# Kernel optimization log

Measured on AMD Instinct MI355X. Metric: run time of the kernel, lower is better.

The kernel has to match this reference:

```python
import jax, jax.numpy as jnp
import numpy as np

H = 256    # hidden_size
NH = 8     # num_heads
B = 256    # batch_size (num graphs)
M = 128    # max_num_nodes per graph
N = B * M  # total nodes
E = N * 16 # total edges


def _bn(x, g, b, eps=1e-5):
    # BatchNorm1d in training mode: batch stats over node dim, biased variance
    m = x.mean(0)
    v = ((x - m) ** 2).mean(0)
    return g * (x - m) * jax.lax.rsqrt(v + eps) + b


def setup_inputs() -> dict:
    key = jax.random.key(0)
    ks = jax.random.split(key, 12)
    def lin(k, o, i):
        return jax.random.normal(k, (o, i), jnp.float32) / np.sqrt(i).astype(np.float32)
    return {
        "h": jax.random.normal(ks[0], (N, H), jnp.float32),
        "gin_w1": lin(ks[1], H, H), "gin_b1": jnp.zeros((H,), jnp.float32),
        "gin_w2": lin(ks[2], H, H), "gin_b2": jnp.zeros((H,), jnp.float32),
        "in_proj_w": lin(ks[3], 3 * H, H), "in_proj_b": jnp.zeros((3 * H,), jnp.float32),
        "out_proj_w": lin(ks[4], H, H), "out_proj_b": jnp.zeros((H,), jnp.float32),
        "bn_local_g": jnp.ones((H,), jnp.float32), "bn_local_b": jnp.zeros((H,), jnp.float32),
        "bn_attn_g": jnp.ones((H,), jnp.float32), "bn_attn_b": jnp.zeros((H,), jnp.float32),
        "bn_out_g": jnp.ones((H,), jnp.float32), "bn_out_b": jnp.zeros((H,), jnp.float32),
        "ffn1_w": lin(ks[5], 2 * H, H), "ffn1_b": jnp.zeros((2 * H,), jnp.float32),
        "ffn2_w": lin(ks[6], H, 2 * H), "ffn2_b": jnp.zeros((H,), jnp.float32),
        "edge_src": jax.random.randint(ks[7], (E,), 0, N, dtype=jnp.int32),
        "edge_dst": jax.random.randint(ks[8], (E,), 0, N, dtype=jnp.int32),
        "batch_num_nodes": jnp.full((B,), M, dtype=jnp.int32),
    }


def reference(h, gin_w1, gin_b1, gin_w2, gin_b2, in_proj_w, in_proj_b,
              out_proj_w, out_proj_b, bn_local_g, bn_local_b, bn_attn_g, bn_attn_b,
              bn_out_g, bn_out_b, ffn1_w, ffn1_b, ffn2_w, ffn2_b,
              edge_src, edge_dst, batch_num_nodes):
    # ---- local GIN conv: gin_nn((1+eps)*h + sum_neighbors h), eps=0 ----
    agg = jax.ops.segment_sum(h[edge_src], edge_dst, num_segments=N)
    z = h + agg
    z = jax.nn.relu(z @ gin_w1.T + gin_b1) @ gin_w2.T + gin_b2
    h_local = _bn(h + z, bn_local_g, bn_local_b)  # dropout=0

    # ---- to_dense_batch scatter indices ----
    cum = jnp.concatenate([jnp.zeros((1,), batch_num_nodes.dtype), jnp.cumsum(batch_num_nodes)])
    node = jnp.arange(N, dtype=jnp.int32)
    bid = jnp.searchsorted(cum[1:], node, side='right')  # graph id per node
    idx = node - cum[bid] + bid * M                      # slot in dense [B*M]
    hd = jnp.zeros((B * M, H), h.dtype).at[idx].set(h).reshape(B, M, H)
    mask = jnp.zeros((B * M,), bool).at[idx].set(True).reshape(B, M)

    # ---- MultiheadAttention (batch_first, self-attn, key_padding_mask) ----
    qkv = hd @ in_proj_w.T + in_proj_b
    q, k, v = jnp.split(qkv, 3, axis=-1)
    dh = H // NH
    q = q.reshape(B, M, NH, dh)
    k = k.reshape(B, M, NH, dh)
    v = v.reshape(B, M, NH, dh)
    scores = jnp.einsum('bqhd,bkhd->bhqk', q, k) / np.float32(np.sqrt(dh))
    scores = jnp.where(mask[:, None, None, :], scores, jnp.float32(-1e9))
    attn = jax.nn.softmax(scores, axis=-1)
    ao = jnp.einsum('bhqk,bkhd->bqhd', attn, v).reshape(B, M, H)
    ao = ao @ out_proj_w.T + out_proj_b
    h_attn = ao.reshape(B * M, H)[idx]  # ragged gather back (x[mask])
    h_attn = _bn(h + h_attn, bn_attn_g, bn_attn_b)

    # ---- combine + FFN + out norm ----
    hh = h_local + h_attn
    hh = hh + (jax.nn.relu(hh @ ffn1_w.T + ffn1_b) @ ffn2_w.T + ffn2_b)
    return _bn(hh, bn_out_g, bn_out_b)
```

## Files before the change

kernel.cpp:

```cpp
#include <hip/hip_runtime.h>

#define NNODES 32768
#define HDIM   256
#define NHEADS 8
#define NB     256
#define NEDGES 524288


typedef unsigned short u16;
typedef unsigned int   u32;
typedef unsigned long long u64;
typedef __attribute__((ext_vector_type(8))) short short8;
typedef __attribute__((ext_vector_type(4))) float f32x4;

__device__ __forceinline__ float bf2f(u16 u){
  union { u32 i; float f; } x; x.i = ((u32)u) << 16; return x.f;
}
__device__ __forceinline__ u16 f2bf(float f){
  union { float f; u32 i; } x; x.f = f;
  u32 r = x.i + 0x7fffu + ((x.i >> 16) & 1u);
  return (u16)(r >> 16);
}
__device__ __forceinline__ void unpack8(uint4 v, float* f){
  f[0] = bf2f((u16)(v.x & 0xffff)); f[1] = bf2f((u16)(v.x >> 16));
  f[2] = bf2f((u16)(v.y & 0xffff)); f[3] = bf2f((u16)(v.y >> 16));
  f[4] = bf2f((u16)(v.z & 0xffff)); f[5] = bf2f((u16)(v.z >> 16));
  f[6] = bf2f((u16)(v.w & 0xffff)); f[7] = bf2f((u16)(v.w >> 16));
}
__device__ __forceinline__ uint4 pack8(const float* f){
  uint4 v;
  v.x = (u32)f2bf(f[0]) | ((u32)f2bf(f[1]) << 16);
  v.y = (u32)f2bf(f[2]) | ((u32)f2bf(f[3]) << 16);
  v.z = (u32)f2bf(f[4]) | ((u32)f2bf(f[5]) << 16);
  v.w = (u32)f2bf(f[6]) | ((u32)f2bf(f[7]) << 16);
  return v;
}

typedef __attribute__((address_space(3))) unsigned int lds_u32;
typedef const __attribute__((address_space(1))) unsigned int gbl_u32;
__device__ __forceinline__ void gload16(const void* g, void* l){
  __builtin_amdgcn_global_load_lds((gbl_u32*)(u64)g,
                                   (lds_u32*)(u32)(u64)l, 16, 0, 0);
}

struct CvtPtrs { const void* p[19]; };

__device__ static const int CVT_CH[19] = {
  2097152,16384,64,16384,64,49152,192,16384,64,64,64,64,64,64,64,32768,128,32768,64};
__device__ static const int CVT_PR[19] = {
  0,8388608,8454144,8454400,8519936,8520192,8716800,8717568,8783104,
  8783360,8783616,8783872,8784128,8784384,8784640,8784896,8915968,8916480,9047552};
#define CVT_TOTAL_CHUNKS 2261952

__global__ __launch_bounds__(256) void convert_k(CvtPtrs cp, u16* __restrict__ dst,
    const int* __restrict__ edge_dst, int* __restrict__ counts){
  int gid = blockIdx.x * 256 + threadIdx.x;
  if (gid < NEDGES) atomicAdd(&counts[edge_dst[gid]], 1);
  if (gid >= CVT_TOTAL_CHUNKS) return;
  int t = 0, rem = gid;
  while (t < 18 && rem >= CVT_CH[t]) { rem -= CVT_CH[t]; t++; }
  u16* d = dst + CVT_PR[t] + (size_t)rem * 4;
  float4 v = ((const float4*)cp.p[t])[rem];
  u16 o[4] = { f2bf(v.x), f2bf(v.y), f2bf(v.z), f2bf(v.w) };
  *(uint2*)d = *(const uint2*)o;
}

__global__ void scan_k(const int* __restrict__ counts, int* __restrict__ offsets,
                       int* __restrict__ cursor, float* __restrict__ stats,
                       int nzero){
  __shared__ int part[1024];
  int t = threadIdx.x;
  for (int i = t; i < nzero; i += 1024) stats[i] = 0.0f;
  int local[32];
  int s = 0;
  int base = t * 32;
#pragma unroll
  for (int i = 0; i < 32; i++){ local[i] = counts[base + i]; s += local[i]; }
  part[t] = s;
  __syncthreads();
  for (int off = 1; off < 1024; off <<= 1){
    int v = (t >= off) ? part[t - off] : 0;
    __syncthreads();
    part[t] += v;
    __syncthreads();
  }
  int run = part[t] - s;
#pragma unroll
  for (int i = 0; i < 32; i++){
    offsets[base + i] = run; cursor[base + i] = run; run += local[i];
  }
  if (t == 1023) offsets[NNODES] = run;
}

__global__ void bucket_k(const int* __restrict__ src, const int* __restrict__ dst,
                         int* __restrict__ cursor, int* __restrict__ srcs){
  int e = blockIdx.x * 256 + threadIdx.x;
  int p = atomicAdd(&cursor[dst[e]], 1);
  srcs[p] = src[e];
}

__global__ __launch_bounds__(256) void agg_k(const u16* __restrict__ h,
    const int* __restrict__ offsets, const int* __restrict__ srcs,
    u16* __restrict__ z0){
  int node = blockIdx.x * 4 + (threadIdx.x >> 6);
  int lane = threadIdx.x & 63;
  size_t coff = (size_t)lane * 4;
  int beg = offsets[node], end = offsets[node + 1];

  uint2 self = *(const uint2*)&h[(size_t)node * HDIM + coff];
  float a0 = bf2f((u16)(self.x & 0xffff)), a1 = bf2f((u16)(self.x >> 16));
  float a2 = bf2f((u16)(self.y & 0xffff)), a3 = bf2f((u16)(self.y >> 16));

  int e = beg;
  for (; e + 8 <= end; e += 8){
    uint2 v[8];
#pragma unroll
    for (int i = 0; i < 8; i++){
      int s = srcs[e + i];
      v[i] = *(const uint2*)&h[(size_t)s * HDIM + coff];
    }
#pragma unroll
    for (int i = 0; i < 8; i++){
      a0 += bf2f((u16)(v[i].x & 0xffff));
      a1 += bf2f((u16)(v[i].x >> 16));
      a2 += bf2f((u16)(v[i].y & 0xffff));
      a3 += bf2f((u16)(v[i].y >> 16));
    }
  }
  for (; e < end; e++){
    int s = srcs[e];
    uint2 va = *(const uint2*)&h[(size_t)s * HDIM + coff];
    a0 += bf2f((u16)(va.x & 0xffff));
    a1 += bf2f((u16)(va.x >> 16));
    a2 += bf2f((u16)(va.y & 0xffff));
    a3 += bf2f((u16)(va.y >> 16));
  }

  uint2 o;
  o.x = (u32)f2bf(a0) | ((u32)f2bf(a1) << 16);
  o.y = (u32)f2bf(a2) | ((u32)f2bf(a3) << 16);
  *(uint2*)&z0[(size_t)node * HDIM + coff] = o;
}

__device__ __forceinline__ void mfma_step(const u16* AS_, const u16* WS_,
    f32x4 (&acc)[4][4], int wm, int wn, int ln, int qs){
  short8 af[4], bfr[4];
#pragma unroll
  for (int mt = 0; mt < 4; mt++)
    af[mt] = *(const short8*)&AS_[(wm * 64 + mt * 16 + ln) * 32 + qs];
#pragma unroll
  for (int nt = 0; nt < 4; nt++)
    bfr[nt] = *(const short8*)&WS_[(wn * 64 + nt * 16 + ln) * 32 + qs];
#pragma unroll
  for (int mt = 0; mt < 4; mt++)
#pragma unroll
    for (int nt = 0; nt < 4; nt++)
      acc[mt][nt] = __builtin_amdgcn_mfma_f32_16x16x32_bf16(af[mt], bfr[nt], acc[mt][nt], 0, 0, 0);
}

template<int K>
__device__ __forceinline__ void kloop(const u16* __restrict__ A,
    const u16* __restrict__ W, u16* smem, int m0, int n0, int tid,
    f32x4 (&acc)[4][4]){
  u16* As0 = smem;        u16* Ws0 = smem + 4096;
  u16* As1 = smem + 8192; u16* Ws1 = smem + 12288;
  const int wave = tid >> 6, lane = tid & 63;
  const int wm = wave >> 1, wn = wave & 1;
  const int ln = lane & 15, q4 = lane >> 4;
  const int qs = (q4 ^ ((ln >> 1) & 3)) << 3;
  const int r_l = tid >> 2;
  const int csw = ((tid & 3) ^ ((tid >> 3) & 3)) << 3;
  const u16* gA = A + (size_t)(m0 + r_l) * K + csw;
  const u16* gW = W + (size_t)(n0 + r_l) * K + csw;
  u16* dA0 = As0 + wave * 512; u16* dW0 = Ws0 + wave * 512;
  u16* dA1 = As1 + wave * 512; u16* dW1 = Ws1 + wave * 512;
  const int NT = K / 32;

  gload16(gA, dA0); gload16(gA + 64 * K, dA0 + 2048);
  gload16(gW, dW0); gload16(gW + 64 * K, dW0 + 2048);
  __syncthreads();

#pragma unroll
  for (int t = 0; t < NT; t += 2){
    if (t + 1 < NT){
      int kn = (t + 1) * 32;
      gload16(gA + kn, dA1); gload16(gA + 64 * K + kn, dA1 + 2048);
      gload16(gW + kn, dW1); gload16(gW + 64 * K + kn, dW1 + 2048);
    }
    mfma_step(As0, Ws0, acc, wm, wn, ln, qs);
    __syncthreads();
    if (t + 2 < NT){
      int kn = (t + 2) * 32;
      gload16(gA + kn, dA0); gload16(gA + 64 * K + kn, dA0 + 2048);
      gload16(gW + kn, dW0); gload16(gW + 64 * K + kn, dW0 + 2048);
    }
    mfma_step(As1, Ws1, acc, wm, wn, ln, qs);
    __syncthreads();
  }
}

struct GemmCfg {
  const u16* A; const u16* W; const u16* bias; const u16* res;
  u16* C; float* ssum; float* ssq;
  int NO; int nx; int relu; int sh;
};

__device__ __forceinline__ void remap(int f, int nx, int& m0, int& n0){
  int xcd = f & 7, j = f >> 3;
  m0 = (xcd + ((j / nx) << 3)) << 7;
  n0 = (j % nx) << 7;
}

template<bool RES, bool STATS>
__device__ __forceinline__ void epilogue(f32x4 (&acc)[4][4], u16* smem,
    const GemmCfg& c, int m0, int n0, int tid, int shoff){
  const int NO = c.NO;
  const int wave = tid >> 6, lane = tid & 63;
  const int wm = wave >> 1, wn = wave & 1;
  const int q4 = lane >> 4, ln = lane & 15;

  if (RES){
#pragma unroll
    for (int i = 0; i < 8; i++){
      int ch = tid + i * 256;
      int r = ch >> 4, k = ch & 15;
      uint4 vv = *(const uint4*)&c.res[(size_t)(m0 + r) * NO + n0 + (k << 3)];
      *(uint4*)&smem[r * 128 + ((((k >> 1) ^ (r & 7)) << 4)) + ((k & 1) << 3)] = vv;
    }
    __syncthreads();
  }

#pragma unroll
  for (int nt = 0; nt < 4; nt++){
    int lcol = wn * 64 + nt * 16 + ln;
    int gcol = n0 + lcol;
    float bv = bf2f(c.bias[gcol]);
    int chunk = lcol >> 4;
    float cs = 0.0f, cq = 0.0f;
#pragma unroll
    for (int mt = 0; mt < 4; mt++){
      int lrow = wm * 64 + mt * 16 + q4 * 4;
#pragma unroll
      for (int reg = 0; reg < 4; reg++){
        int r = lrow + reg;
        int sidx = r * 128 + ((chunk ^ (r & 7)) << 4) + ln;
        float v = acc[mt][nt][reg] + bv;
        if (c.relu) v = fmaxf(v, 0.0f);
        if (RES) v += bf2f(smem[sidx]);
        smem[sidx] = f2bf(v);
        if (STATS){ cs += v; cq += v * v; }
      }
    }
    if (STATS){
      cs += __shfl_xor(cs, 16); cs += __shfl_xor(cs, 32);
      cq += __shfl_xor(cq, 16); cq += __shfl_xor(cq, 32);
      if (lane < 16){
        atomicAdd(&c.ssum[shoff + gcol], cs);
        atomicAdd(&c.ssq[shoff + gcol], cq);
      }
    }
  }
  __syncthreads();

#pragma unroll
  for (int i = 0; i < 8; i++){
    int ch = tid + i * 256;
    int r = ch >> 4, k = ch & 15;
    uint4 vv = *(const uint4*)&smem[r * 128 + (((k >> 1) ^ (r & 7)) << 4) + ((k & 1) << 3)];
    *(uint4*)&c.C[(size_t)(m0 + r) * NO + n0 + (k << 3)] = vv;
  }
}

template<int K, bool RES, bool STATS>
__global__ __launch_bounds__(256) void gemm_one(GemmCfg c){
  __shared__ u16 smem[16384];
  const int tid = threadIdx.x;
  int m0, n0; remap(blockIdx.x, c.nx, m0, n0);
  f32x4 acc[4][4] = {};
  kloop<K>(c.A, c.W, smem, m0, n0, tid, acc);
  epilogue<RES, STATS>(acc, smem, c, m0, n0, tid, (blockIdx.x & c.sh) * 1536);
}

template<bool RES, bool STATS>
__global__ __launch_bounds__(256) void gemm_dual(GemmCfg c0, GemmCfg c1, int split){
  __shared__ u16 smem[16384];
  const int tid = threadIdx.x;
  const int fid = blockIdx.x;
  GemmCfg c = (fid < split) ? c0 : c1;
  int f = (fid < split) ? fid : fid - split;
  int m0, n0; remap(f, c.nx, m0, n0);
  f32x4 acc[4][4] = {};
  kloop<256>(c.A, c.W, smem, m0, n0, tid, acc);
  epilogue<RES, STATS>(acc, smem, c, m0, n0, tid, (f & c.sh) * 1536);
}

__global__ __launch_bounds__(256) void attn_k(const u16* __restrict__ qkv,
                                              u16* __restrict__ ao){
  __shared__ u16 sm[21760];
  u16* VTs = sm;
  u16* Qs  = sm + 4352;
  u16* Ks  = sm + 9472;
  u16* Ps  = sm + 4352;

  const int b  = blockIdx.x >> 3;
  const int nh = blockIdx.x & 7;
  const int tid = threadIdx.x;
  const int wave = tid >> 6, lane = tid & 63;
  const int q4 = lane >> 4, ln = lane & 15;

#pragma unroll
  for (int c2 = 0; c2 < 2; c2++){
    int chunk = tid + c2 * 256;
    int r = chunk >> 2;
    int cc = chunk & 3;
    size_t nb = (size_t)(b * 128 + r) * 768 + nh * 32 + cc * 8;
    uint4 vq = *(const uint4*)&qkv[nb];
    uint4 vk = *(const uint4*)&qkv[nb + 256];
    uint4 vv = *(const uint4*)&qkv[nb + 512];
    *(uint4*)&Qs[r * 40 + cc * 8] = vq;
    *(uint4*)&Ks[r * 40 + cc * 8] = vk;
    union { uint4 v; u16 h[8]; } uv; uv.v = vv;
#pragma unroll
    for (int i = 0; i < 8; i++) VTs[(cc * 8 + i) * 136 + r] = uv.h[i];
  }
  __syncthreads();

  f32x4 accs[2][8] = {};
  short8 qf[2];
#pragma unroll
  for (int mt = 0; mt < 2; mt++)
    qf[mt] = *(const short8*)&Qs[(wave * 32 + mt * 16 + ln) * 40 + q4 * 8];
#pragma unroll
  for (int nt = 0; nt < 8; nt++){
    short8 kf = *(const short8*)&Ks[(nt * 16 + ln) * 40 + q4 * 8];
    accs[0][nt] = __builtin_amdgcn_mfma_f32_16x16x32_bf16(qf[0], kf, accs[0][nt], 0, 0, 0);
    accs[1][nt] = __builtin_amdgcn_mfma_f32_16x16x32_bf16(qf[1], kf, accs[1][nt], 0, 0, 0);
  }

  const float scale = 0.17677669529663687f;
  float invs[2][4];
#pragma unroll
  for (int mt = 0; mt < 2; mt++){
#pragma unroll
    for (int reg = 0; reg < 4; reg++){
      float rm = -1e30f;
#pragma unroll
      for (int nt = 0; nt < 8; nt++){
        accs[mt][nt][reg] *= scale;
        rm = fmaxf(rm, accs[mt][nt][reg]);
      }
      for (int m = 1; m < 16; m <<= 1) rm = fmaxf(rm, __shfl_xor(rm, m));
      float rs = 0.0f;
#pragma unroll
      for (int nt = 0; nt < 8; nt++){
        float e = __expf(accs[mt][nt][reg] - rm);
        accs[mt][nt][reg] = e;
        rs += e;
      }
      for (int m = 1; m < 16; m <<= 1) rs += __shfl_xor(rs, m);
      invs[mt][reg] = 1.0f / rs;
    }
  }

  __syncthreads();
#pragma unroll
  for (int mt = 0; mt < 2; mt++)
#pragma unroll
    for (int nt = 0; nt < 8; nt++)
#pragma unroll
      for (int reg = 0; reg < 4; reg++)
        Ps[(wave * 32 + mt * 16 + q4 * 4 + reg) * 136 + nt * 16 + ln] =
            f2bf(accs[mt][nt][reg] * invs[mt][reg]);
  __syncthreads();

  f32x4 acco[2][2] = {};
#pragma unroll
  for (int kk = 0; kk < 4; kk++){
    short8 pf[2], vf[2];
#pragma unroll
    for (int mt = 0; mt < 2; mt++)
      pf[mt] = *(const short8*)&Ps[(wave * 32 + mt * 16 + ln) * 136 + kk * 32 + q4 * 8];
#pragma unroll
    for (int nt = 0; nt < 2; nt++)
      vf[nt] = *(const short8*)&VTs[(nt * 16 + ln) * 136 + kk * 32 + q4 * 8];
#pragma unroll
    for (int mt = 0; mt < 2; mt++)
#pragma unroll
      for (int nt = 0; nt < 2; nt++)
        acco[mt][nt] = __builtin_amdgcn_mfma_f32_16x16x32_bf16(pf[mt], vf[nt], acco[mt][nt], 0, 0, 0);
  }

  __syncthreads();
  u16* Os = Ps;
#pragma unroll
  for (int mt = 0; mt < 2; mt++)
#pragma unroll
    for (int nt = 0; nt < 2; nt++)
#pragma unroll
      for (int reg = 0; reg < 4; reg++)
        Os[(wave * 32 + mt * 16 + q4 * 4 + reg) * 40 + nt * 16 + ln] =
            f2bf(acco[mt][nt][reg]);
  __syncthreads();
#pragma unroll
  for (int i = 0; i < 2; i++){
    int ch = tid + i * 256;
    int r = ch >> 2, k = ch & 3;
    uint4 vv = *(const uint4*)&Os[r * 40 + k * 8];
    *(uint4*)&ao[(size_t)(b * 128 + r) * HDIM + nh * 32 + k * 8] = vv;
  }
}

__global__ __launch_bounds__(256) void combine_k(const u16* __restrict__ xl,
    const u16* __restrict__ xa, const float* __restrict__ stats, int ns,
    const u16* __restrict__ gl, const u16* __restrict__ bl,
    const u16* __restrict__ ga, const u16* __restrict__ ba,
    u16* __restrict__ hh){
  __shared__ float cs0[256], cs1[256], cs2[256];
  int t = threadIdx.x;
  {
    float s0 = 0.f, s1 = 0.f, s2 = 0.f, s3 = 0.f;
    for (int s = 0; s < ns; s++){
      const float* sb = stats + s * 1536;
      s0 += sb[t]; s1 += sb[256 + t]; s2 += sb[512 + t]; s3 += sb[768 + t];
    }
    const float invN = 1.0f / 32768.0f;
    float mA = s0 * invN;
    float vA = s1 * invN - mA * mA;
    float sA = bf2f(gl[t]) * rsqrtf(vA + 1e-5f);
    float tA = bf2f(bl[t]) - mA * sA;
    float mB = s2 * invN;
    float vB = s3 * invN - mB * mB;
    float sB = bf2f(ga[t]) * rsqrtf(vB + 1e-5f);
    float tB = bf2f(ba[t]) - mB * sB;
    cs0[t] = sA; cs1[t] = sB; cs2[t] = tA + tB;
  }
  __syncthreads();
  int gid = blockIdx.x * 256 + t;
  size_t off = (size_t)gid * 8;
  int cb = (int)(off & 255);
  float sl[8], sa[8], tt[8];
  *(float4*)&sl[0] = *(const float4*)&cs0[cb];
  *(float4*)&sl[4] = *(const float4*)&cs0[cb + 4];
  *(float4*)&sa[0] = *(const float4*)&cs1[cb];
  *(float4*)&sa[4] = *(const float4*)&cs1[cb + 4];
  *(float4*)&tt[0] = *(const float4*)&cs2[cb];
  *(float4*)&tt[4] = *(const float4*)&cs2[cb + 4];
  float fl[8], fa[8], fo[8];
  unpack8(*(const uint4*)&xl[off], fl);
  unpack8(*(const uint4*)&xa[off], fa);
#pragma unroll
  for (int i = 0; i < 8; i++) fo[i] = sl[i] * fl[i] + sa[i] * fa[i] + tt[i];
  *(uint4*)&hh[off] = pack8(fo);
}

__global__ __launch_bounds__(256) void finalbn_k(const u16* __restrict__ y,
    const float* __restrict__ stats, int ns, const u16* __restrict__ g,
    const u16* __restrict__ bb, float* __restrict__ out){
  __shared__ float cs0[256], cs1[256];
  int t = threadIdx.x;
  {
    float s0 = 0.f, s1 = 0.f;
    for (int s = 0; s < ns; s++){
      const float* sb = stats + s * 1536;
      s0 += sb[1024 + t]; s1 += sb[1280 + t];
    }
    const float invN = 1.0f / 32768.0f;
    float m = s0 * invN;
    float v = s1 * invN - m * m;
    float sc = bf2f(g[t]) * rsqrtf(v + 1e-5f);
    cs0[t] = sc; cs1[t] = bf2f(bb[t]) - m * sc;
  }
  __syncthreads();
  int gid = blockIdx.x * 256 + t;
  size_t off = (size_t)gid * 8;
  int cb = (int)(off & 255);
  float ss[8], tt[8];
  *(float4*)&ss[0] = *(const float4*)&cs0[cb];
  *(float4*)&ss[4] = *(const float4*)&cs0[cb + 4];
  *(float4*)&tt[0] = *(const float4*)&cs1[cb];
  *(float4*)&tt[4] = *(const float4*)&cs1[cb + 4];
  float fy[8], fo[8];
  unpack8(*(const uint4*)&y[off], fy);
#pragma unroll
  for (int i = 0; i < 8; i++) fo[i] = ss[i] * fy[i] + tt[i];
  *(float4*)&out[off] = *(const float4*)&fo[0];
  *(float4*)&out[off + 4] = *(const float4*)&fo[4];
}

extern "C" void kernel_launch(void* const* d_in, const int* in_sizes, int n_in,
                              void* d_out, int out_size, void* d_ws, size_t ws_size,
                              hipStream_t stream){
  const int* edge_src = (const int*)d_in[19];
  const int* edge_dst = (const int*)d_in[20];

  char* ws = (char*)d_ws;
  float* stats = (float*)ws;
  u16*   conv  = (u16*)(ws + 12288);
  u16*   A     = (u16*)(ws + 12288 + 18095616);
  u16*   Bb    = (u16*)(ws + 12288 + 18095616 + 16777216);
  u16*   C     = (u16*)d_out;
  const size_t BIG_NEED = 51662336ull + 50331648ull + 49152ull;
  const bool big = (ws_size >= BIG_NEED);
  u16* QKV = (u16*)(ws + 51662336);
  float* SH = (float*)(ws + 101993984);

  float* sbase = big ? SH : stats;
  const int smask = big ? 7 : 0;
  const int nshard = smask + 1;

  int* counts  = (int*)Bb;
  int* offsets = (int*)((char*)Bb + 131072);
  int* cursor  = (int*)((char*)Bb + 262400);
  int* srcs    = (int*)((char*)Bb + 393472);

  const u16* convH = conv;
  const u16* W1  = conv + 8388608; const u16* b1g = conv + 8454144;
  const u16* W2  = conv + 8454400; const u16* b2g = conv + 8519936;
  const u16* Win = conv + 8520192; const u16* bin = conv + 8716800;
  const u16* Wo  = conv + 8717568; const u16* bo  = conv + 8783104;
  const u16* g_l = conv + 8783360; const u16* b_l = conv + 8783616;
  const u16* g_a = conv + 8783872; const u16* b_a = conv + 8784128;
  const u16* g_o = conv + 8784384; const u16* b_o = conv + 8784640;
  const u16* Wf1 = conv + 8784896; const u16* bf1 = conv + 8915968;
  const u16* Wf2 = conv + 8916480; const u16* bf2 = conv + 9047552;

  hipMemsetAsync(counts, 0, 131072, stream);

  CvtPtrs cp;
  for (int i = 0; i < 19; i++) cp.p[i] = d_in[i];
  convert_k<<<8836, 256, 0, stream>>>(cp, conv, edge_dst, counts);

  scan_k<<<1, 1024, 0, stream>>>(counts, offsets, cursor, sbase, nshard * 1536);
  bucket_k<<<NEDGES / 256, 256, 0, stream>>>(edge_src, edge_dst, cursor, srcs);
  agg_k<<<NNODES / 4, 256, 0, stream>>>(convH, offsets, srcs, A);

  if (big){
    GemmCfg cg1  = { A,     W1,  b1g, nullptr, Bb,  nullptr, nullptr, 256, 2, 1, 0 };
    GemmCfg cqkv = { convH, Win, bin, nullptr, QKV, nullptr, nullptr, 768, 6, 0, 0 };
    gemm_dual<false, false><<<512 + 1536, 256, 0, stream>>>(cg1, cqkv, 512);

    attn_k<<<2048, 256, 0, stream>>>(QKV, C);

    u16* XA = QKV;
    GemmCfg cg2 = { Bb, W2, b2g, convH, A,  sbase + 0,   sbase + 256, 256, 2, 0, smask };
    GemmCfg cop = { C,  Wo, bo,  convH, XA, sbase + 512, sbase + 768, 256, 2, 0, smask };
    gemm_dual<true, true><<<1024, 256, 0, stream>>>(cg2, cop, 512);

    combine_k<<<4096, 256, 0, stream>>>(A, XA, sbase, nshard, g_l, b_l, g_a, b_a, C);
  } else {
    GemmCfg cg1 = { A, W1, b1g, nullptr, Bb, nullptr, nullptr, 256, 2, 1, 0 };
    gemm_one<256, false, false><<<512, 256, 0, stream>>>(cg1);
    GemmCfg cg2 = { Bb, W2, b2g, convH, A, sbase + 0, sbase + 256, 256, 2, 0, smask };
    gemm_one<256, true, true><<<512, 256, 0, stream>>>(cg2);
    for (int c = 0; c < 4; c++){
      const u16* hA = convH + (size_t)c * 8192 * HDIM;
      u16* aoC = C + (size_t)c * 8192 * HDIM;
      GemmCfg cq = { hA, Win, bin, nullptr, Bb, nullptr, nullptr, 768, 6, 0, 0 };
      gemm_one<256, false, false><<<384, 256, 0, stream>>>(cq);
      attn_k<<<512, 256, 0, stream>>>(Bb, aoC);
    }
    GemmCfg cop = { C, Wo, bo, convH, Bb, sbase + 512, sbase + 768, 256, 2, 0, smask };
    gemm_one<256, true, true><<<512, 256, 0, stream>>>(cop);
    combine_k<<<4096, 256, 0, stream>>>(A, Bb, sbase, nshard, g_l, b_l, g_a, b_a, C);
  }

  GemmCfg cf1 = { C, Wf1, bf1, nullptr, A, nullptr, nullptr, 512, 4, 1, 0 };
  gemm_one<256, false, false><<<1024, 256, 0, stream>>>(cf1);
  GemmCfg cf2 = { A, Wf2, bf2, C, (u16*)conv, sbase + 1024, sbase + 1280, 256, 2, 0, smask };
  gemm_one<512, true, true><<<512, 256, 0, stream>>>(cf2);

  finalbn_k<<<4096, 256, 0, stream>>>(conv, sbase, nshard, g_o, b_o, (float*)d_out);
}
```

Before: 381.9 us.

## Co-schedule edge aggregation with QKV GEMM and GIN GEMM1 with attention

Reorders the dependency schedule so independent work shares a single launch. Edge aggregation now runs inside the QKV projection GEMM kernel via a block-index split. The first GIN GEMM runs alongside the attention kernel in another combined launch. This is meant to fill idle compute units and cut launch and tail gaps between stages; in exchange, the combined kernels carry the larger shared-memory footprint, which may lower occupancy for the GEMM blocks, and the fallback path computes a QKV result it then overwrites.

Result: slower. 404.2 us (+5.8%).

```diff
diff --git a/kernel.cpp b/kernel.cpp
--- a/kernel.cpp
+++ b/kernel.cpp
@@ -99,11 +99,9 @@
   srcs[p] = src[e];
 }
 
-__global__ __launch_bounds__(256) void agg_k(const u16* __restrict__ h,
-    const int* __restrict__ offsets, const int* __restrict__ srcs,
-    u16* __restrict__ z0){
-  int node = blockIdx.x * 4 + (threadIdx.x >> 6);
-  int lane = threadIdx.x & 63;
+__device__ __forceinline__ void agg_body(int node, int lane,
+    const u16* __restrict__ h, const int* __restrict__ offsets,
+    const int* __restrict__ srcs, u16* __restrict__ z0){
   size_t coff = (size_t)lane * 4;
   int beg = offsets[node], end = offsets[node + 1];
 
@@ -294,17 +292,32 @@
   epilogue<RES, STATS>(acc, smem, c, m0, n0, tid, (f & c.sh) * 1536);
 }
 
-__global__ __launch_bounds__(256) void attn_k(const u16* __restrict__ qkv,
-                                              u16* __restrict__ ao){
-  __shared__ u16 sm[21760];
+__global__ __launch_bounds__(256) void aggqkv_k(GemmCfg cq,
+    const u16* __restrict__ h, const int* __restrict__ offsets,
+    const int* __restrict__ srcs, u16* __restrict__ z0){
+  __shared__ u16 smem[16384];
+  const int fid = blockIdx.x;
+  const int tid = threadIdx.x;
+  if (fid < 1536){
+    int m0, n0; remap(fid, cq.nx, m0, n0);
+    f32x4 acc[4][4] = {};
+    kloop<256>(cq.A, cq.W, smem, m0, n0, tid, acc);
+    epilogue<false, false>(acc, smem, cq, m0, n0, tid, 0);
+  } else {
+    int node = (fid - 1536) * 4 + (tid >> 6);
+    agg_body(node, tid & 63, h, offsets, srcs, z0);
+  }
+}
+
+__device__ __forceinline__ void attn_body(u16* sm, int bid,
+    const u16* __restrict__ qkv, u16* __restrict__ ao, int tid){
   u16* VTs = sm;
   u16* Qs  = sm + 4352;
   u16* Ks  = sm + 9472;
   u16* Ps  = sm + 4352;
 
-  const int b  = blockIdx.x >> 3;
-  const int nh = blockIdx.x & 7;
-  const int tid = threadIdx.x;
+  const int b  = bid >> 3;
+  const int nh = bid & 7;
   const int wave = tid >> 6, lane = tid & 63;
   const int q4 = lane >> 4, ln = lane & 15;
 
@@ -407,6 +420,27 @@
     int r = ch >> 2, k = ch & 3;
     uint4 vv = *(const uint4*)&Os[r * 40 + k * 8];
     *(uint4*)&ao[(size_t)(b * 128 + r) * HDIM + nh * 32 + k * 8] = vv;
+  }
+}
+
+__global__ __launch_bounds__(256) void attn_k(const u16* __restrict__ qkv,
+                                              u16* __restrict__ ao){
+  __shared__ u16 sm[21760];
+  attn_body(sm, blockIdx.x, qkv, ao, threadIdx.x);
+}
+
+__global__ __launch_bounds__(256) void g1attn_k(GemmCfg c1,
+    const u16* __restrict__ qkv, u16* __restrict__ ao){
+  __shared__ u16 sm[21760];
+  const int fid = blockIdx.x;
+  const int tid = threadIdx.x;
+  if (fid < 512){
+    int m0, n0; remap(fid, c1.nx, m0, n0);
+    f32x4 acc[4][4] = {};
+    kloop<256>(c1.A, c1.W, sm, m0, n0, tid, acc);
+    epilogue<false, false>(acc, sm, c1, m0, n0, tid, 0);
+  } else {
+    attn_body(sm, fid - 512, qkv, ao, tid);
   }
 }
 
@@ -532,14 +566,13 @@
 
   scan_k<<<1, 1024, 0, stream>>>(counts, offsets, cursor, sbase, nshard * 1536);
   bucket_k<<<NEDGES / 256, 256, 0, stream>>>(edge_src, edge_dst, cursor, srcs);
-  agg_k<<<NNODES / 4, 256, 0, stream>>>(convH, offsets, srcs, A);
 
   if (big){
-    GemmCfg cg1  = { A,     W1,  b1g, nullptr, Bb,  nullptr, nullptr, 256, 2, 1, 0 };
     GemmCfg cqkv = { convH, Win, bin, nullptr, QKV, nullptr, nullptr, 768, 6, 0, 0 };
-    gemm_dual<false, false><<<512 + 1536, 256, 0, stream>>>(cg1, cqkv, 512);
-
-    attn_k<<<2048, 256, 0, stream>>>(QKV, C);
+    aggqkv_k<<<1536 + 8192, 256, 0, stream>>>(cqkv, convH, offsets, srcs, A);
+
+    GemmCfg cg1 = { A, W1, b1g, nullptr, Bb, nullptr, nullptr, 256, 2, 1, 0 };
+    g1attn_k<<<512 + 2048, 256, 0, stream>>>(cg1, QKV, C);
 
     u16* XA = QKV;
     GemmCfg cg2 = { Bb, W2, b2g, convH, A,  sbase + 0,   sbase + 256, 256, 2, 0, smask };
@@ -548,6 +581,9 @@
 
     combine_k<<<4096, 256, 0, stream>>>(A, XA, sbase, nshard, g_l, b_l, g_a, b_a, C);
   } else {
+    aggqkv_k<<<1536 + 8192, 256, 0, stream>>>(
+        GemmCfg{ convH, Win, bin, nullptr, Bb, nullptr, nullptr, 768, 6, 0, 0 },
+        convH, offsets, srcs, A);
     GemmCfg cg1 = { A, W1, b1g, nullptr, Bb, nullptr, nullptr, 256, 2, 1, 0 };
     gemm_one<256, false, false><<<512, 256, 0, stream>>>(cg1);
     GemmCfg cg2 = { Bb, W2, b2g, convH, A, sbase + 0, sbase + 256, 256, 2, 0, smask };
```
